# Kernel tuning notes

Measured on AMD Instinct MI355X. Metric: run time of the kernel, lower is better.

The kernel has to match this reference:

```python
import jax, jax.numpy as jnp
import numpy as np

WH, WW = 16, 16
NUM_HEADS = 16
DIM = 1024
BATCH = 64
SEQ = WH * WW + 1  # 257, includes cls token
NUM_REL = (2 * WH - 1) * (2 * WW - 1) + 3  # 964


def _make_rel_pos_index(wh, ww):
    # BEiT relative position index construction (intended semantics of the torch code)
    coords = np.stack(np.meshgrid(np.arange(wh), np.arange(ww), indexing='ij'))  # [2, wh, ww]
    flat = coords.reshape(2, -1)  # [2, wh*ww]
    rel = flat[:, :, None] - flat[:, None, :]  # [2, N-1, N-1]
    rel = rel.transpose(1, 2, 0).astype(np.int64)
    rel[:, :, 0] += wh - 1
    rel[:, :, 1] += ww - 1
    rel[:, :, 0] *= 2 * ww - 1
    num_rel = (2 * wh - 1) * (2 * ww - 1) + 3
    idx = np.zeros((wh * ww + 1, wh * ww + 1), dtype=np.int32)
    idx[1:, 1:] = rel.sum(-1)
    idx[0, :] = num_rel - 3  # cls-to-token
    idx[:, 0] = num_rel - 2  # token-to-cls
    idx[0, 0] = num_rel - 1  # cls-to-cls
    return idx


def setup_inputs() -> dict:
    key = jax.random.key(0)
    ks = jax.random.split(key, 7)
    return {
        'x': jax.random.normal(ks[0], (BATCH, SEQ, DIM), dtype=jnp.float32),
        'qkv_weight': jax.random.normal(ks[1], (3 * DIM, DIM), dtype=jnp.float32) * 0.02,
        'query_bias': jax.random.normal(ks[2], (DIM,), dtype=jnp.float32) * 0.02,
        'value_bias': jax.random.normal(ks[3], (DIM,), dtype=jnp.float32) * 0.02,
        'rel_pos_bias_table': jax.random.normal(ks[4], (NUM_REL, NUM_HEADS), dtype=jnp.float32) * 0.02,
        'proj_weight': jax.random.normal(ks[5], (DIM, DIM), dtype=jnp.float32) * 0.02,
        'proj_bias': jax.random.normal(ks[6], (DIM,), dtype=jnp.float32) * 0.02,
        'rel_pos_index': jnp.asarray(_make_rel_pos_index(WH, WW)),
    }


def reference(x, qkv_weight, query_bias, value_bias, rel_pos_bias_table,
              proj_weight, proj_bias, rel_pos_index):
    B, N, C = x.shape
    H = rel_pos_bias_table.shape[-1]
    D = qkv_weight.shape[0] // 3 // H
    scale = D ** -0.5
    # qkv bias: (q_bias, zeros, v_bias) as in the torch module
    qkv_bias = jnp.concatenate([query_bias, jnp.zeros_like(value_bias), value_bias])
    qkv = x @ qkv_weight.T + qkv_bias  # [B, N, 3*H*D]
    qkv = qkv.reshape(B, N, 3, H, D).transpose(2, 0, 3, 1, 4)  # [3, B, H, N, D]
    q, k, v = qkv[0] * scale, qkv[1], qkv[2]
    attn = jnp.einsum('bhqd,bhkd->bhqk', q, k)  # [B, H, N, N]
    bias = rel_pos_bias_table[rel_pos_index]  # [N, N, H]
    attn = attn + bias.transpose(2, 0, 1)[None]  # add per-head bias
    attn = jax.nn.softmax(attn, axis=-1)
    out = jnp.einsum('bhqk,bhkd->bhqd', attn, v)  # [B, H, N, D]
    out = out.transpose(0, 2, 1, 3).reshape(B, N, H * D)
    return out @ proj_weight.T + proj_bias
```

## Files before the change

### kernel.cpp

```cpp
#include <hip/hip_runtime.h>


typedef unsigned short u16;
typedef __attribute__((ext_vector_type(8))) short bf16x8;
typedef __attribute__((ext_vector_type(4))) float f32x4;

#define MFMA16(a, b, c) __builtin_amdgcn_mfma_f32_16x16x32_bf16(a, b, c, 0, 0, 0)
#define GLDS16(g, l)                                                           \
  __builtin_amdgcn_global_load_lds(                                            \
      (const __attribute__((address_space(1))) void*)(g),                      \
      (__attribute__((address_space(3))) void*)(l), 16, 0, 0)

#define QOFF 0
#define KOFF 16842752
#define VTOFF 33685504
#define VTP 264

__device__ __forceinline__ u16 f2bf(float f) {
  unsigned u = __builtin_bit_cast(unsigned, f);
  u += 0x7FFFu + ((u >> 16) & 1u);
  return (u16)(u >> 16);
}
__device__ __forceinline__ unsigned pack2(float a, float b) {
  return (unsigned)f2bf(a) | ((unsigned)f2bf(b) << 16);
}

__global__ __launch_bounds__(256) void cvt_bf16(const float* __restrict__ in,
                                                u16* __restrict__ out, int n4) {
  int i = blockIdx.x * 256 + threadIdx.x;
  if (i < n4) {
    float4 v = ((const float4*)in)[i];
    uint2 o;
    o.x = pack2(v.x, v.y);
    o.y = pack2(v.z, v.w);
    ((uint2*)out)[i] = o;
  }
}

__global__ __launch_bounds__(256) void bias_pre(const float* __restrict__ tab,
                                                const int* __restrict__ idx,
                                                u16* __restrict__ out) {
  int t = blockIdx.x * 256 + threadIdx.x;
  if (t < 66049) {
    int i = t / 257, j = t - i * 257;
    int off = i * 288 + ((j >> 5) << 5) + ((j & 15) << 1) + ((j >> 4) & 1);
    int id = idx[t];
    const float* row = tab + (size_t)id * 16;
#pragma unroll
    for (int h = 0; h < 16; h++)
      out[(size_t)h * 74016 + off] = f2bf(row[h] * 1.4426950408889634f);
  } else if (t < 66049 + 257 * 31) {
    int u = t - 66049;
    int i = u / 31, j = 257 + (u - i * 31);
    int off = i * 288 + ((j >> 5) << 5) + ((j & 15) << 1) + ((j >> 4) & 1);
#pragma unroll
    for (int h = 0; h < 16; h++)
      out[(size_t)h * 74016 + off] = 0xFF7Fu;
  }
}


#define GSTAGE(BO, TI)                                                         \
  GLDS16(pa0 + (TI) * 32, SMEM + (BO) + tid * 8);                              \
  GLDS16(pa1 + (TI) * 32, SMEM + (BO) + 2048 + tid * 8);                       \
  GLDS16(pb0 + (TI) * 32, SMEM + (BO) + 4096 + tid * 8);                       \
  GLDS16(pb1 + (TI) * 32, SMEM + (BO) + 6144 + tid * 8);

#define GCOMPUTE(BO)                                                           \
  {                                                                            \
    const u16* As_ = SMEM + (BO);                                              \
    const u16* Bs_ = SMEM + (BO) + 4096;                                       \
    bf16x8 bfr[4];                                                             \
    _Pragma("unroll") for (int t = 0; t < 4; t++)                              \
        bfr[t] = *(const bf16x8*)(Bs_ + (wc + t * 16 + l15) * 32 + fo);        \
    _Pragma("unroll") for (int i = 0; i < 4; i++) {                            \
      bf16x8 afr = *(const bf16x8*)(As_ + (wr + i * 16 + l15) * 32 + fo);      \
      _Pragma("unroll") for (int j = 0; j < 4; j++)                            \
          acc[i][j] = MFMA16(afr, bfr[j], acc[i][j]);                          \
    }                                                                          \
  }

#define GEMM_PROLOG(M_, K_)                                                    \
  __shared__ __align__(16) u16 SMEM[16384];                                    \
  const int M = (M_), K = (K_);                                                \
  const int tid = threadIdx.x;                                                 \
  const int lane = tid & 63, wave = tid >> 6;                                  \
  const int quad = lane >> 4, l15 = lane & 15;                                 \
  const int wr = (wave >> 1) * 64, wc = (wave & 1) * 64;                       \
  const int m0 = blockIdx.y * 128, n0 = blockIdx.x * 128;                      \
  const int sgk = (((tid & 3) ^ ((tid >> 3) & 3))) * 8;  \
  const int fo = ((quad ^ ((l15 >> 1) & 3))) * 8;         \
  const u16* pa0 = A + (size_t)(m0 + (tid >> 2)) * K + sgk;                    \
  const u16* pa1 = pa0 + (size_t)64 * K;                                       \
  const u16* pb0 = B + (size_t)(n0 + (tid >> 2)) * K + sgk;                    \
  const u16* pb1 = pb0 + (size_t)64 * K;                                       \
  f32x4 acc[4][4];                                                             \
  _Pragma("unroll") for (int i = 0; i < 4; i++)                                \
  _Pragma("unroll") for (int j = 0; j < 4; j++)                                \
      acc[i][j] = (f32x4){0.f, 0.f, 0.f, 0.f};                                 \
  GSTAGE(0, 0)                                                                 \
  __syncthreads();                                                             \
  for (int kt = 0; kt < 30; kt += 2) {                                         \
    GSTAGE(8192, kt + 1)                                                       \
    GCOMPUTE(0)                                                                \
    __syncthreads();                                                           \
    GSTAGE(0, kt + 2)                                                          \
    GCOMPUTE(8192)                                                             \
    __syncthreads();                                                           \
  }                                                                            \
  GSTAGE(8192, 31)                                                             \
  GCOMPUTE(0)                                                                  \
  __syncthreads();                                                             \
  GCOMPUTE(8192)

__global__ __launch_bounds__(256, 4) void gemm_qkv(
    const u16* __restrict__ A, const u16* __restrict__ B,
    const float* __restrict__ qbias, const float* __restrict__ vbias,
    u16* __restrict__ C) {
  GEMM_PROLOG(16448, 1024)
  if (n0 >= 2048) {
    u16* const T = SMEM;
    for (int p = 0; p < 2; p++) {
      __syncthreads();
      if ((wave & 1) == p) {
#pragma unroll
        for (int j = 0; j < 4; j++) {
          int cl = j * 16 + l15;
          int rem = (n0 + wc + j * 16 + l15) & 1023;
          float vb_ = vbias[rem];
          int swz = (cl & 15) << 3;
#pragma unroll
          for (int i = 0; i < 4; i++) {
            int rlb = wr + i * 16 + quad * 4;
#pragma unroll
            for (int rr = 0; rr < 2; rr++) {
              unsigned pk = pack2(acc[i][j][rr * 2] + vb_,
                                  acc[i][j][rr * 2 + 1] + vb_);
              *(unsigned*)(T + cl * 128 + ((rlb + rr * 2) ^ swz)) = pk;
            }
          }
        }
      }
      __syncthreads();
#pragma unroll
      for (int cc = 0; cc < 16; cc++) {
        int cl = cc * 4 + wave;
        int rem = (n0 + p * 64 + cl) & 1023;
        int h = rem >> 6, d = rem & 63;
        size_t cb = (size_t)VTOFF + ((size_t)h * 64 + d) * VTP;
        int swz = (cl & 15) << 3;
#pragma unroll
        for (int half = 0; half < 2; half++) {
          int rl = half * 64 + lane;
          u16 val = T[cl * 128 + (rl ^ swz)];
          int m = m0 + rl;
          if (m < M) {
            unsigned bb2 = (unsigned)m / 257u;
            unsigned nn2 = (unsigned)m - bb2 * 257u;
            C[cb + (size_t)bb2 * (16 * 64 * VTP) + nn2] = val;
          }
        }
      }
    }
  } else {
#pragma unroll
    for (int i = 0; i < 4; i++) {
#pragma unroll
      for (int r = 0; r < 4; r++) {
        int row = m0 + wr + i * 16 + quad * 4 + r;
        if (row < M) {
          unsigned bb = (unsigned)row / 257u;
          unsigned nn = (unsigned)row - bb * 257u;
#pragma unroll
          for (int j = 0; j < 4; j++) {
            int c = n0 + wc + j * 16 + l15;
            int which = c >> 10, rem = c & 1023;
            float bias = (which == 0) ? qbias[rem] : 0.f;
            float v = acc[i][j][r] + bias;
            if (which == 0) v *= 0.18033688011112042f;
            int h = rem >> 6, d = rem & 63;
            size_t dst = (size_t)which * 16842752 +
                         (size_t)(bb * 16 + h) * 16448 + (size_t)nn * 64 + d;
            C[dst] = f2bf(v);
          }
        }
      }
    }
  }
}

__global__ __launch_bounds__(256, 4) void gemm_proj(
    const u16* __restrict__ A, const u16* __restrict__ B,
    const float* __restrict__ pbias, float* __restrict__ C) {
  GEMM_PROLOG(16448, 1024)
#pragma unroll
  for (int i = 0; i < 4; i++) {
#pragma unroll
    for (int r = 0; r < 4; r++) {
      int row = m0 + wr + i * 16 + quad * 4 + r;
      if (row < M) {
#pragma unroll
        for (int j = 0; j < 4; j++) {
          int c = n0 + wc + j * 16 + l15;
          C[(size_t)row * 1024 + c] = acc[i][j][r] + pbias[c];
        }
      }
    }
  }
}

__global__ __launch_bounds__(256, 3) void attn_fused(
    const u16* __restrict__ qkv, const u16* __restrict__ biasT,
    u16* __restrict__ out) {
  __shared__ __align__(16) u16 KVs[96 * 72];
  __shared__ __align__(16) u16 Ps[4 * 16 * 104];
  const int bx = blockIdx.x;
  const int xj = bx & 7, xi = bx >> 3;
  const int qt = xi % 5;
  const int bh = (xi / 5) * 8 + xj;
  const int b = bh >> 4, h = bh & 15;
  const int tid = threadIdx.x, lane = tid & 63, wave = tid >> 6;
  const int quad = lane >> 4, l15 = lane & 15;
  const bool act = (qt < 4) || (wave == 0);
  const u16* qg = qkv + QOFF + (size_t)bh * 16448;
  const u16* kg = qkv + KOFF + (size_t)bh * 16448;
  const u16* vtg = qkv + VTOFF + (size_t)bh * (64 * VTP);

  int qra = qt * 64 + wave * 16 + l15;
  if (qra > 256) qra = 256;
  const bf16x8 aq0 = *(const bf16x8*)(qg + (size_t)qra * 64 + quad * 8);
  const bf16x8 aq1 = *(const bf16x8*)(qg + (size_t)qra * 64 + 32 + quad * 8);

  const int qbase = qt * 64 + wave * 16 + quad * 4;
  f32x4 s[18];
  if (act) {
    const u16* bb = biasT + (size_t)h * 74016;
#pragma unroll
    for (int r = 0; r < 4; r++) {
      int qr = qbase + r;
      if (qr > 256) qr = 256;
      const unsigned* brow = (const unsigned*)(bb + (size_t)qr * 288);
#pragma unroll
      for (int p = 0; p < 9; p++) {
        unsigned u = brow[p * 16 + l15];
        s[2 * p][r] = __builtin_bit_cast(float, u << 16);
        s[2 * p + 1][r] = __builtin_bit_cast(float, u & 0xFFFF0000u);
      }
    }
  }

  const bf16x8 zv = {0, 0, 0, 0, 0, 0, 0, 0};
  for (int ck = 0; ck < 3; ck++) {
    __syncthreads();
#pragma unroll
    for (int it = 0; it < 3; it++) {
      int g = it * 256 + tid;
      int row = g >> 3, col = (g & 7) * 8;
      int gr = ck * 96 + row;
      bf16x8 kv = (gr < 257) ? *(const bf16x8*)(kg + (size_t)gr * 64 + col) : zv;
      *(bf16x8*)(KVs + row * 72 + col) = kv;
    }
    __syncthreads();
    if (act) {
#pragma unroll
      for (int nt = 0; nt < 6; nt++) {
        bf16x8 b0 = *(const bf16x8*)(KVs + (nt * 16 + l15) * 72 + quad * 8);
        bf16x8 b1 = *(const bf16x8*)(KVs + (nt * 16 + l15) * 72 + 32 + quad * 8);
        int t = ck * 6 + nt;
        s[t] = MFMA16(aq0, b0, s[t]);
        s[t] = MFMA16(aq1, b1, s[t]);
      }
    }
  }

  float inv[4];
  if (act) {
#pragma unroll
    for (int r = 0; r < 4; r++) {
      float m = -3e38f;
#pragma unroll
      for (int t = 0; t < 18; t++) m = fmaxf(m, s[t][r]);
      m = fmaxf(m, __shfl_xor(m, 1));
      m = fmaxf(m, __shfl_xor(m, 2));
      m = fmaxf(m, __shfl_xor(m, 4));
      m = fmaxf(m, __shfl_xor(m, 8));
      float sum = 0.f;
#pragma unroll
      for (int t = 0; t < 18; t++) {
        float p = __builtin_amdgcn_exp2f(s[t][r] - m);
        s[t][r] = p;
        sum += p;
      }
      sum += __shfl_xor(sum, 1);
      sum += __shfl_xor(sum, 2);
      sum += __shfl_xor(sum, 4);
      sum += __shfl_xor(sum, 8);
      inv[r] = 1.f / sum;
    }
  }

  u16* Pw = Ps + wave * (16 * 104);
  f32x4 o[4];
#pragma unroll
  for (int nt = 0; nt < 4; nt++) o[nt] = (f32x4){0.f, 0.f, 0.f, 0.f};
  for (int ck = 0; ck < 3; ck++) {
    __syncthreads();
#pragma unroll
    for (int it = 0; it < 3; it++) {
      int g = it * 256 + tid;
      int row = g / 12, c = (g % 12) * 8;
      bf16x8 v = *(const bf16x8*)(vtg + (size_t)row * VTP + ck * 96 + c);
      *(bf16x8*)(KVs + row * 104 + c) = v;
    }
    if (act) {
#pragma unroll
      for (int nt = 0; nt < 6; nt++) {
        int t = ck * 6 + nt;
#pragma unroll
        for (int r = 0; r < 4; r++)
          Pw[(quad * 4 + r) * 104 + nt * 16 + l15] = f2bf(s[t][r]);
      }
    }
    __syncthreads();
    if (act) {
#pragma unroll
      for (int ks = 0; ks < 3; ks++) {
        bf16x8 ap = *(const bf16x8*)(Pw + l15 * 104 + ks * 32 + quad * 8);
#pragma unroll
        for (int nt = 0; nt < 4; nt++) {
          bf16x8 bv =
              *(const bf16x8*)(KVs + (nt * 16 + l15) * 104 + ks * 32 + quad * 8);
          o[nt] = MFMA16(ap, bv, o[nt]);
        }
      }
    }
  }

  if (act) {
#pragma unroll
    for (int nt = 0; nt < 4; nt++) {
      int d = nt * 16 + l15;
#pragma unroll
      for (int r = 0; r < 4; r++) {
        int qr = qbase + r;
        if (qr < 257)
          out[((size_t)b * 257 + qr) * 1024 + h * 64 + d] =
              f2bf(o[nt][r] * inv[r]);
      }
    }
  }
}

extern "C" void kernel_launch(void* const* d_in, const int* in_sizes, int n_in,
                              void* d_out, int out_size, void* d_ws,
                              size_t ws_size, hipStream_t stream) {
  const float* x = (const float*)d_in[0];
  const float* qkvw = (const float*)d_in[1];
  const float* qb = (const float*)d_in[2];
  const float* vb = (const float*)d_in[3];
  const float* tab = (const float*)d_in[4];
  const float* pw = (const float*)d_in[5];
  const float* pb = (const float*)d_in[6];
  const int* rpi = (const int*)d_in[7];

  char* ws = (char*)d_ws;
  u16* qkvbuf = (u16*)ws;
  u16* xbuf = (u16*)(ws + 101974016);
  u16* biasb = (u16*)(ws + 135659520);
  u16* qkvwb = (u16*)(ws + 139886656);
  u16* projwb = (u16*)(ws + 146178112);

  cvt_bf16<<<16448, 256, 0, stream>>>(x, xbuf, 4210688);
  cvt_bf16<<<3072, 256, 0, stream>>>(qkvw, qkvwb, 786432);
  cvt_bf16<<<1024, 256, 0, stream>>>(pw, projwb, 262144);
  bias_pre<<<290, 256, 0, stream>>>(tab, rpi, biasb);
  gemm_qkv<<<dim3(24, 129), 256, 0, stream>>>(xbuf, qkvwb, qb, vb, qkvbuf);
  attn_fused<<<5120, 256, 0, stream>>>(qkvbuf, biasb, xbuf);
  gemm_proj<<<dim3(8, 129), 256, 0, stream>>>(xbuf, projwb, pb, (float*)d_out);
}
```

Measured before the change: 407.2 us.

## Prefetch K/V chunks into registers in attention and use BK=64 QKV GEMM

```diff
diff --git a/kernel.cpp b/kernel.cpp
--- a/kernel.cpp
+++ b/kernel.cpp
@@ -59,6 +59,42 @@
   }
 }
 
+#define GEMM_PROLOG64(M_, K_)                                                  \
+  __shared__ __align__(16) u16 SMEM[16384];                                    \
+  const int M = (M_), K = (K_);                                                \
+  const int tid = threadIdx.x;                                                 \
+  const int lane = tid & 63, wave = tid >> 6;                                  \
+  const int quad = lane >> 4, l15 = lane & 15;                                 \
+  const int wr = (wave >> 1) * 64, wc = (wave & 1) * 64;                       \
+  const int m0 = blockIdx.y * 128, n0 = blockIdx.x * 128;                      \
+  const int sgk = ((tid & 7) ^ ((tid >> 3) & 7)) * 8;                          \
+  const int fo0 = (quad ^ (l15 & 7)) * 8;                                      \
+  const int fo1 = ((4 + quad) ^ (l15 & 7)) * 8;                                \
+  const u16* pa0 = A + (size_t)(m0 + (tid >> 3)) * K + sgk;                    \
+  const u16* pb0 = B + (size_t)(n0 + (tid >> 3)) * K + sgk;                    \
+  f32x4 acc[4][4];                                                             \
+  _Pragma("unroll") for (int i = 0; i < 4; i++)                                \
+  _Pragma("unroll") for (int j = 0; j < 4; j++)                                \
+      acc[i][j] = (f32x4){0.f, 0.f, 0.f, 0.f};                                 \
+  for (int k0 = 0; k0 < K; k0 += 64) {                                         \
+    __syncthreads();                                                           \
+    _Pragma("unroll") for (int b = 0; b < 4; b++) {                            \
+      GLDS16(pa0 + k0 + (size_t)b * 32 * K, SMEM + b * 2048 + tid * 8);        \
+      GLDS16(pb0 + k0 + (size_t)b * 32 * K, SMEM + 8192 + b * 2048 + tid * 8); \
+    }                                                                          \
+    __syncthreads();                                                           \
+    _Pragma("unroll") for (int kk = 0; kk < 2; kk++) {                         \
+      const int fo = kk ? fo1 : fo0;                                           \
+      bf16x8 bfr[4];                                                           \
+      _Pragma("unroll") for (int t = 0; t < 4; t++)                            \
+          bfr[t] = *(const bf16x8*)(SMEM + 8192 + (wc + t * 16 + l15) * 64 + fo); \
+      _Pragma("unroll") for (int i = 0; i < 4; i++) {                          \
+        bf16x8 afr = *(const bf16x8*)(SMEM + (wr + i * 16 + l15) * 64 + fo);   \
+        _Pragma("unroll") for (int j = 0; j < 4; j++)                          \
+            acc[i][j] = MFMA16(afr, bfr[j], acc[i][j]);                        \
+      }                                                                        \
+    }                                                                          \
+  }
 
 #define GSTAGE(BO, TI)                                                         \
   GLDS16(pa0 + (TI) * 32, SMEM + (BO) + tid * 8);                              \
@@ -80,7 +116,7 @@
     }                                                                          \
   }
 
-#define GEMM_PROLOG(M_, K_)                                                    \
+#define GEMM_PROLOG_DB(M_, K_)                                                 \
   __shared__ __align__(16) u16 SMEM[16384];                                    \
   const int M = (M_), K = (K_);                                                \
   const int tid = threadIdx.x;                                                 \
@@ -88,8 +124,8 @@
   const int quad = lane >> 4, l15 = lane & 15;                                 \
   const int wr = (wave >> 1) * 64, wc = (wave & 1) * 64;                       \
   const int m0 = blockIdx.y * 128, n0 = blockIdx.x * 128;                      \
-  const int sgk = (((tid & 3) ^ ((tid >> 3) & 3))) * 8;  \
-  const int fo = ((quad ^ ((l15 >> 1) & 3))) * 8;         \
+  const int sgk = (((tid & 3) ^ ((tid >> 3) & 3))) * 8;                        \
+  const int fo = ((quad ^ ((l15 >> 1) & 3))) * 8;                              \
   const u16* pa0 = A + (size_t)(m0 + (tid >> 2)) * K + sgk;                    \
   const u16* pa1 = pa0 + (size_t)64 * K;                                       \
   const u16* pb0 = B + (size_t)(n0 + (tid >> 2)) * K + sgk;                    \
@@ -117,7 +153,7 @@
     const u16* __restrict__ A, const u16* __restrict__ B,
     const float* __restrict__ qbias, const float* __restrict__ vbias,
     u16* __restrict__ C) {
-  GEMM_PROLOG(16448, 1024)
+  GEMM_PROLOG64(16448, 1024)
   if (n0 >= 2048) {
     u16* const T = SMEM;
     for (int p = 0; p < 2; p++) {
@@ -192,7 +228,7 @@
 __global__ __launch_bounds__(256, 4) void gemm_proj(
     const u16* __restrict__ A, const u16* __restrict__ B,
     const float* __restrict__ pbias, float* __restrict__ C) {
-  GEMM_PROLOG(16448, 1024)
+  GEMM_PROLOG_DB(16448, 1024)
 #pragma unroll
   for (int i = 0; i < 4; i++) {
 #pragma unroll
@@ -208,6 +244,61 @@
     }
   }
 }
+
+#define KLOAD(d0, d1, d2, CK)                                                  \
+  {                                                                            \
+    int gr0 = (CK) * 96 + r0;                                                  \
+    d0 = (gr0 < 257) ? *(const bf16x8*)(kg + (size_t)gr0 * 64 + c0) : zv;      \
+    d1 = (gr0 + 32 < 257) ? *(const bf16x8*)(kg + (size_t)(gr0 + 32) * 64 + c0) : zv; \
+    d2 = (gr0 + 64 < 257) ? *(const bf16x8*)(kg + (size_t)(gr0 + 64) * 64 + c0) : zv; \
+  }
+#define KWRITE(s0, s1, s2)                                                     \
+  {                                                                            \
+    *(bf16x8*)(KVs + r0 * 72 + c0) = s0;                                       \
+    *(bf16x8*)(KVs + (r0 + 32) * 72 + c0) = s1;                                \
+    *(bf16x8*)(KVs + (r0 + 64) * 72 + c0) = s2;                                \
+  }
+#define VLOAD(d0, d1, d2, CK)                                                  \
+  {                                                                            \
+    d0 = *(const bf16x8*)(vtg + (size_t)vr0 * VTP + (CK) * 96 + vc0);          \
+    d1 = *(const bf16x8*)(vtg + (size_t)vr1 * VTP + (CK) * 96 + vc1);          \
+    d2 = *(const bf16x8*)(vtg + (size_t)vr2 * VTP + (CK) * 96 + vc2);          \
+  }
+#define VWRITE(s0, s1, s2)                                                     \
+  {                                                                            \
+    *(bf16x8*)(KVs + vr0 * 104 + vc0) = s0;                                    \
+    *(bf16x8*)(KVs + vr1 * 104 + vc1) = s1;                                    \
+    *(bf16x8*)(KVs + vr2 * 104 + vc2) = s2;                                    \
+  }
+#define QKMFMA(CK)                                                             \
+  if (act) {                                                                   \
+    _Pragma("unroll") for (int nt = 0; nt < 6; nt++) {                         \
+      bf16x8 b0 = *(const bf16x8*)(KVs + (nt * 16 + l15) * 72 + quad * 8);     \
+      bf16x8 b1 = *(const bf16x8*)(KVs + (nt * 16 + l15) * 72 + 32 + quad * 8);\
+      int t = (CK) * 6 + nt;                                                   \
+      s[t] = MFMA16(aq0, b0, s[t]);                                            \
+      s[t] = MFMA16(aq1, b1, s[t]);                                            \
+    }                                                                          \
+  }
+#define PWRITE(CK)                                                             \
+  if (act) {                                                                   \
+    _Pragma("unroll") for (int nt = 0; nt < 6; nt++) {                         \
+      int t = (CK) * 6 + nt;                                                   \
+      _Pragma("unroll") for (int r = 0; r < 4; r++)                            \
+          Pw[(quad * 4 + r) * 104 + nt * 16 + l15] = f2bf(s[t][r]);            \
+    }                                                                          \
+  }
+#define PVMFMA                                                                 \
+  if (act) {                                                                   \
+    _Pragma("unroll") for (int ks = 0; ks < 3; ks++) {                         \
+      bf16x8 ap = *(const bf16x8*)(Pw + l15 * 104 + ks * 32 + quad * 8);       \
+      _Pragma("unroll") for (int nt = 0; nt < 4; nt++) {                       \
+        bf16x8 bv =                                                            \
+            *(const bf16x8*)(KVs + (nt * 16 + l15) * 104 + ks * 32 + quad * 8);\
+        o[nt] = MFMA16(ap, bv, o[nt]);                                         \
+      }                                                                        \
+    }                                                                          \
+  }
 
 __global__ __launch_bounds__(256, 3) void attn_fused(
     const u16* __restrict__ qkv, const u16* __restrict__ biasT,
@@ -226,6 +317,15 @@
   const u16* kg = qkv + KOFF + (size_t)bh * 16448;
   const u16* vtg = qkv + VTOFF + (size_t)bh * (64 * VTP);
 
+  const int r0 = tid >> 3, c0 = (tid & 7) * 8;
+  const int vr0 = tid / 12, vc0 = (tid % 12) * 8;
+  const int vr1 = (256 + tid) / 12, vc1 = ((256 + tid) % 12) * 8;
+  const int vr2 = (512 + tid) / 12, vc2 = ((512 + tid) % 12) * 8;
+  const bf16x8 zv = {0, 0, 0, 0, 0, 0, 0, 0};
+
+  bf16x8 kva0, kva1, kva2, kvb0, kvb1, kvb2;
+  KLOAD(kva0, kva1, kva2, 0)
+
   int qra = qt * 64 + wave * 16 + l15;
   if (qra > 256) qra = 256;
   const bf16x8 aq0 = *(const bf16x8*)(qg + (size_t)qra * 64 + quad * 8);
@@ -249,29 +349,21 @@
     }
   }
 
-  const bf16x8 zv = {0, 0, 0, 0, 0, 0, 0, 0};
-  for (int ck = 0; ck < 3; ck++) {
-    __syncthreads();
-#pragma unroll
-    for (int it = 0; it < 3; it++) {
-      int g = it * 256 + tid;
-      int row = g >> 3, col = (g & 7) * 8;
-      int gr = ck * 96 + row;
-      bf16x8 kv = (gr < 257) ? *(const bf16x8*)(kg + (size_t)gr * 64 + col) : zv;
-      *(bf16x8*)(KVs + row * 72 + col) = kv;
-    }
-    __syncthreads();
-    if (act) {
-#pragma unroll
-      for (int nt = 0; nt < 6; nt++) {
-        bf16x8 b0 = *(const bf16x8*)(KVs + (nt * 16 + l15) * 72 + quad * 8);
-        bf16x8 b1 = *(const bf16x8*)(KVs + (nt * 16 + l15) * 72 + 32 + quad * 8);
-        int t = ck * 6 + nt;
-        s[t] = MFMA16(aq0, b0, s[t]);
-        s[t] = MFMA16(aq1, b1, s[t]);
-      }
-    }
-  }
+  __syncthreads();
+  KWRITE(kva0, kva1, kva2)
+  KLOAD(kvb0, kvb1, kvb2, 1)
+  __syncthreads();
+  QKMFMA(0)
+  __syncthreads();
+  KWRITE(kvb0, kvb1, kvb2)
+  KLOAD(kva0, kva1, kva2, 2)
+  __syncthreads();
+  QKMFMA(1)
+  __syncthreads();
+  KWRITE(kva0, kva1, kva2)
+  VLOAD(kvb0, kvb1, kvb2, 0)
+  __syncthreads();
+  QKMFMA(2)
 
   float inv[4];
   if (act) {
@@ -303,38 +395,23 @@
   f32x4 o[4];
 #pragma unroll
   for (int nt = 0; nt < 4; nt++) o[nt] = (f32x4){0.f, 0.f, 0.f, 0.f};
-  for (int ck = 0; ck < 3; ck++) {
-    __syncthreads();
-#pragma unroll
-    for (int it = 0; it < 3; it++) {
-      int g = it * 256 + tid;
-      int row = g / 12, c = (g % 12) * 8;
-      bf16x8 v = *(const bf16x8*)(vtg + (size_t)row * VTP + ck * 96 + c);
-      *(bf16x8*)(KVs + row * 104 + c) = v;
-    }
-    if (act) {
-#pragma unroll
-      for (int nt = 0; nt < 6; nt++) {
-        int t = ck * 6 + nt;
-#pragma unroll
-        for (int r = 0; r < 4; r++)
-          Pw[(quad * 4 + r) * 104 + nt * 16 + l15] = f2bf(s[t][r]);
-      }
-    }
-    __syncthreads();
-    if (act) {
-#pragma unroll
-      for (int ks = 0; ks < 3; ks++) {
-        bf16x8 ap = *(const bf16x8*)(Pw + l15 * 104 + ks * 32 + quad * 8);
-#pragma unroll
-        for (int nt = 0; nt < 4; nt++) {
-          bf16x8 bv =
-              *(const bf16x8*)(KVs + (nt * 16 + l15) * 104 + ks * 32 + quad * 8);
-          o[nt] = MFMA16(ap, bv, o[nt]);
-        }
-      }
-    }
-  }
+  __syncthreads();
+  VWRITE(kvb0, kvb1, kvb2)
+  VLOAD(kva0, kva1, kva2, 1)
+  PWRITE(0)
+  __syncthreads();
+  PVMFMA
+  __syncthreads();
+  VWRITE(kva0, kva1, kva2)
+  VLOAD(kvb0, kvb1, kvb2, 2)
+  PWRITE(1)
+  __syncthreads();
+  PVMFMA
+  __syncthreads();
+  VWRITE(kvb0, kvb1, kvb2)
+  PWRITE(2)
+  __syncthreads();
+  PVMFMA
 
   if (act) {
 #pragma unroll
```

Measured after the change: 412.5 us. Within noise of the previous version (+1.3%).
